# Kernel tuning notes

Measured on AMD Instinct MI355X. Metric: run time of the kernel, lower is better.

The kernel has to match this reference:

```python
import jax, jax.numpy as jnp
import numpy as np

NUM_HEADS = 16

def setup_inputs() -> dict:
    key = jax.random.key(0)
    ks = jax.random.split(key, 5)
    B, S, H = 16, 1025, 1024
    std = 0.02
    return {
        "hidden_states": jax.random.normal(ks[0], (B, S, H), jnp.float32),
        "w_qkv": jax.random.normal(ks[1], (3 * H, H), jnp.float32) * std,
        "b_qkv": jax.random.normal(ks[2], (3 * H,), jnp.float32) * std,
        "w_dense": jax.random.normal(ks[3], (H, H), jnp.float32) * std,
        "b_dense": jax.random.normal(ks[4], (H,), jnp.float32) * std,
    }

def reference(hidden_states, w_qkv, b_qkv, w_dense, b_dense):
    B, S, H = hidden_states.shape
    nh = NUM_HEADS
    hd = H // nh
    scale = hd ** -0.5
    # fused QKV projection: [B,S,3H]
    mixed = jnp.einsum('bsh,oh->bso', hidden_states, w_qkv) + b_qkv
    # reshape per torch: (B,S,nh,3,hd) -> permute(3,0,2,1,4)
    mixed = mixed.reshape(B, S, nh, 3, hd).transpose(3, 0, 2, 1, 4)
    q, k, v = mixed[0], mixed[1], mixed[2]          # each [B,nh,S,hd]
    scores = jnp.einsum('bhqd,bhkd->bhqk', q, k) * scale
    probs = jax.nn.softmax(scores, axis=-1)          # [B,nh,S,S]
    ctx = jnp.einsum('bhqk,bhkd->bhqd', probs, v)    # [B,nh,S,hd]
    ctx = ctx.transpose(0, 2, 1, 3).reshape(B, S, H)
    out = jnp.einsum('bsh,oh->bso', ctx, w_dense) + b_dense
    return out
```

## Files before the change

kernel.cpp:

```cpp
#include <hip/hip_runtime.h>
#include <math.h>

typedef float f32x4 __attribute__((ext_vector_type(4)));
typedef __bf16 bf16x8 __attribute__((ext_vector_type(8)));
typedef unsigned int u32;
typedef u32 u32x4 __attribute__((ext_vector_type(4)));

#define AS1 __attribute__((address_space(1)))
#define AS3 __attribute__((address_space(3)))

static __device__ __forceinline__ void gload16(const void* g, void* l) {
    __builtin_amdgcn_global_load_lds((const AS1 u32*)g, (AS3 u32*)l, 16, 0, 0);
}
static __device__ __forceinline__ f32x4 mfma16(bf16x8 a, bf16x8 b, f32x4 c) {
    return __builtin_amdgcn_mfma_f32_16x16x32_bf16(a, b, c, 0, 0, 0);
}
static __device__ __forceinline__ float exp2fast(float x) {
    return __builtin_amdgcn_exp2f(x);
}

__global__ __launch_bounds__(256)
void convert_kernel(const float* __restrict__ in, __bf16* __restrict__ out)
{
    const size_t i = ((size_t)blockIdx.x * 256 + threadIdx.x) * 8;
    f32x4 a = *(const f32x4*)(in + i);
    f32x4 b = *(const f32x4*)(in + i + 4);
    bf16x8 o;
    #pragma unroll
    for (int j = 0; j < 4; ++j) { o[j] = (__bf16)a[j]; o[j + 4] = (__bf16)b[j]; }
    *(bf16x8*)(out + i) = o;
}

template<int MODE>
__global__ __launch_bounds__(256)
void gemm_kernel(const __bf16* __restrict__ A, const __bf16* __restrict__ Bw,
                 const float* __restrict__ bias,
                 __bf16* __restrict__ q_out, __bf16* __restrict__ k_out,
                 __bf16* __restrict__ v_out, float* __restrict__ f_out)
{
    constexpr int M = 16400;
    constexpr int K = 1024;

    __shared__ __align__(16) __bf16 As[128 * 64];
    __shared__ __align__(16) __bf16 Bs[128 * 64];

    const int tid  = threadIdx.x;
    const int lane = tid & 63;
    const int wv   = tid >> 6;
    const int wr   = wv >> 1, wc = wv & 1;
    const int fr   = lane & 15, fq = lane >> 4;
    const int m0   = blockIdx.y * 128;
    const int n0   = blockIdx.x * 128;

    const __bf16* aptr[4];
    const __bf16* bptr[4];
    int loff[4];
    #pragma unroll
    for (int qd = 0; qd < 4; ++qd) {
        const int s  = qd * 256 + tid;
        const int r  = s >> 3;
        const int c  = (s & 7) ^ (r & 7);
        loff[qd] = s * 8;
        int ar = m0 + r; if (ar > M - 1) ar = M - 1;
        aptr[qd] = A  + (size_t)ar * K + c * 8;
        bptr[qd] = Bw + (size_t)(n0 + r) * K + c * 8;
    }

    f32x4 acc[4][4];
    #pragma unroll
    for (int i = 0; i < 4; ++i)
        #pragma unroll
        for (int j = 0; j < 4; ++j)
            acc[i][j] = f32x4{0.f, 0.f, 0.f, 0.f};

    for (int kt = 0; kt < K / 64; ++kt) {
        const int kof = kt * 64;
        #pragma unroll
        for (int qd = 0; qd < 4; ++qd) {
            gload16(aptr[qd] + kof, &As[loff[qd]]);
            gload16(bptr[qd] + kof, &Bs[loff[qd]]);
        }
        __syncthreads();

        #pragma unroll
        for (int ks = 0; ks < 2; ++ks) {
            bf16x8 a[4], b[4];
            #pragma unroll
            for (int i = 0; i < 4; ++i) {
                const int ra = wr * 64 + i * 16 + fr;
                const int rb = wc * 64 + i * 16 + fr;
                const int cg = ((ks * 4 + fq) ^ (fr & 7)) * 8;
                a[i] = *(const bf16x8*)&As[ra * 64 + cg];
                b[i] = *(const bf16x8*)&Bs[rb * 64 + cg];
            }
            #pragma unroll
            for (int i = 0; i < 4; ++i)
                #pragma unroll
                for (int j = 0; j < 4; ++j)
                    acc[i][j] = mfma16(a[i], b[j], acc[i][j]);
        }
        __syncthreads();
    }

    #pragma unroll
    for (int ni = 0; ni < 4; ++ni) {
        const int col = n0 + wc * 64 + ni * 16 + fr;
        const float bv = bias[col];
        if constexpr (MODE == 0) {
            const int head = col / 192;
            const int t    = (col >> 6) % 3;
            const int d    = col & 63;
            __bf16* dst = (t == 0) ? q_out : (t == 1 ? k_out : v_out);
            const float scale = (t == 0) ? 0.18033688011112042f : 1.0f;
            #pragma unroll
            for (int mi = 0; mi < 4; ++mi) {
                #pragma unroll
                for (int j = 0; j < 4; ++j) {
                    const int m = m0 + wr * 64 + mi * 16 + fq * 4 + j;
                    if (m < M) {
                        const int bb = m / 1025;
                        const int ss = m - bb * 1025;
                        dst[(((size_t)(bb * 16 + head)) * 1025 + ss) * 64 + d] =
                            (__bf16)((acc[mi][ni][j] + bv) * scale);
                    }
                }
            }
        } else {
            #pragma unroll
            for (int mi = 0; mi < 4; ++mi) {
                #pragma unroll
                for (int j = 0; j < 4; ++j) {
                    const int m = m0 + wr * 64 + mi * 16 + fq * 4 + j;
                    if (m < M) f_out[(size_t)m * 1024 + col] = acc[mi][ni][j] + bv;
                }
            }
        }
    }
}

__global__ __launch_bounds__(256)
void transpose_v(const __bf16* __restrict__ vb, __bf16* __restrict__ vt)
{
    constexpr int S = 1025, S2 = 1088;
    const int bh = blockIdx.y;
    const int s0 = blockIdx.x * 64;
    const int sr = threadIdx.x >> 2, sq = threadIdx.x & 3;
    int srow = s0 + sr; if (srow > S - 1) srow = S - 1;
    const __bf16* src = vb + ((size_t)bh * S + srow) * 64 + sq * 16;
    bf16x8 v0 = *(const bf16x8*)src;
    bf16x8 v1 = *(const bf16x8*)(src + 8);
    __bf16* dst = vt + (size_t)bh * 64 * S2 + s0 + sr;
    #pragma unroll
    for (int i = 0; i < 8; ++i) {
        dst[(size_t)(sq * 16 + i) * S2]     = v0[i];
        dst[(size_t)(sq * 16 + 8 + i) * S2] = v1[i];
    }
}

__global__ __launch_bounds__(256)
void attn_kernel(const __bf16* __restrict__ qb, const __bf16* __restrict__ kb,
                 const __bf16* __restrict__ vtb, __bf16* __restrict__ ctxb)
{
    constexpr int S = 1025, S2 = 1088;
    const int tid  = threadIdx.x;
    const int lane = tid & 63;
    const int w    = tid >> 6;
    const int fr   = lane & 15, fq = lane >> 4;
    const int bh   = blockIdx.y;
    const int q0   = blockIdx.x * 64;
    const int bb   = bh >> 4, hh = bh & 15;

    const __bf16* qp = qb  + (size_t)bh * S * 64;
    const __bf16* kp = kb  + (size_t)bh * S * 64;
    const __bf16* vp = vtb + (size_t)bh * 64 * S2;

    __shared__ __align__(16) __bf16 Ks[64 * 64];
    __shared__ __align__(16) __bf16 Vs[64 * 64];
    __shared__ u32 Ps[4][16 * 33];

    const int s0i = tid, s1i = tid + 256;
    const int r0 = s0i >> 3, g0 = (s0i & 7) ^ (r0 & 7);
    const int r1 = s1i >> 3, g1 = (s1i & 7) ^ (r1 & 7);
    const __bf16* vsrc0 = vp + (size_t)r0 * S2 + g0 * 8;
    const __bf16* vsrc1 = vp + (size_t)r1 * S2 + g1 * 8;

    int qrow = q0 + w * 16 + fr; if (qrow > S - 1) qrow = S - 1;
    const bf16x8 qa0 = *(const bf16x8*)(qp + (size_t)qrow * 64 + fq * 8);
    const bf16x8 qa1 = *(const bf16x8*)(qp + (size_t)qrow * 64 + 32 + fq * 8);

    f32x4 ctx[4];
    #pragma unroll
    for (int di = 0; di < 4; ++di) ctx[di] = f32x4{0.f, 0.f, 0.f, 0.f};
    float mrow = -1e30f;
    float lrow = 0.f;

    u32* psrow_w = &Ps[w][fr * 33];

    for (int kt = 0; kt < 17; ++kt) {
        const int kv0 = kt * 64;
        {
            int kr0 = kv0 + r0; if (kr0 > S - 1) kr0 = S - 1;
            int kr1 = kv0 + r1; if (kr1 > S - 1) kr1 = S - 1;
            gload16(kp + (size_t)kr0 * 64 + g0 * 8, &Ks[s0i * 8]);
            gload16(kp + (size_t)kr1 * 64 + g1 * 8, &Ks[s1i * 8]);
            gload16(vsrc0 + kv0, &Vs[s0i * 8]);
            gload16(vsrc1 + kv0, &Vs[s1i * 8]);
        }
        __syncthreads();

        f32x4 sc[4];
        #pragma unroll
        for (int ni = 0; ni < 4; ++ni) {
            const int row = ni * 16 + fr;
            bf16x8 kf0 = *(const bf16x8*)&Ks[row * 64 + ((fq    ) ^ (row & 7)) * 8];
            bf16x8 kf1 = *(const bf16x8*)&Ks[row * 64 + ((fq + 4) ^ (row & 7)) * 8];
            f32x4 z = f32x4{0.f, 0.f, 0.f, 0.f};
            z = mfma16(kf0, qa0, z);
            sc[ni] = mfma16(kf1, qa1, z);
        }
        if (kv0 + 64 > S) {
            #pragma unroll
            for (int ni = 0; ni < 4; ++ni)
                #pragma unroll
                for (int j = 0; j < 4; ++j)
                    if (kv0 + ni * 16 + fq * 4 + j >= S) sc[ni][j] = -1e30f;
        }

        float mt = sc[0][0];
        #pragma unroll
        for (int ni = 0; ni < 4; ++ni)
            #pragma unroll
            for (int j = 0; j < 4; ++j) mt = fmaxf(mt, sc[ni][j]);
        mt = fmaxf(mt, __shfl_xor(mt, 16, 64));
        mt = fmaxf(mt, __shfl_xor(mt, 32, 64));

        if (__any(mt > mrow + 8.0f)) {
            const float mnew = fmaxf(mrow, mt);
            const float alpha = exp2fast(mrow - mnew);
            mrow = mnew;
            lrow *= alpha;
            float a[4];
            #pragma unroll
            for (int j = 0; j < 4; ++j) a[j] = __shfl(alpha, fq * 4 + j, 64);
            #pragma unroll
            for (int di = 0; di < 4; ++di) {
                ctx[di][0] *= a[0]; ctx[di][1] *= a[1];
                ctx[di][2] *= a[2]; ctx[di][3] *= a[3];
            }
        }

        float p[4][4];
        float s = 0.f;
        #pragma unroll
        for (int ni = 0; ni < 4; ++ni)
            #pragma unroll
            for (int j = 0; j < 4; ++j) {
                p[ni][j] = exp2fast(sc[ni][j] - mrow);
                s += p[ni][j];
            }
        s += __shfl_xor(s, 16, 64);
        s += __shfl_xor(s, 32, 64);
        lrow += s;

        #pragma unroll
        for (int ni = 0; ni < 4; ++ni) {
            #pragma unroll
            for (int h = 0; h < 2; ++h) {
                unsigned short lo = __builtin_bit_cast(unsigned short, (__bf16)p[ni][2 * h]);
                unsigned short hi = __builtin_bit_cast(unsigned short, (__bf16)p[ni][2 * h + 1]);
                psrow_w[fq * 8 + ni * 2 + h] = (u32)lo | ((u32)hi << 16);
            }
        }
        u32x4 pav[2];
        #pragma unroll
        for (int ks = 0; ks < 2; ++ks)
            #pragma unroll
            for (int t = 0; t < 4; ++t) {
                const int slot = (2 * (fq & 1) + (t >> 1)) * 8
                               + (2 * ks + (fq >> 1)) * 2 + (t & 1);
                pav[ks][t] = psrow_w[slot];
            }

        #pragma unroll
        for (int ks = 0; ks < 2; ++ks) {
            const bf16x8 pa = __builtin_bit_cast(bf16x8, pav[ks]);
            #pragma unroll
            for (int di = 0; di < 4; ++di) {
                const int row = di * 16 + fr;
                bf16x8 vf = *(const bf16x8*)&Vs[row * 64 + ((ks * 4 + fq) ^ (row & 7)) * 8];
                ctx[di] = mfma16(pa, vf, ctx[di]);
            }
        }
        __syncthreads();
    }

    float linv[4];
    #pragma unroll
    for (int j = 0; j < 4; ++j) linv[j] = 1.0f / __shfl(lrow, fq * 4 + j, 64);
    #pragma unroll
    for (int di = 0; di < 4; ++di) {
        #pragma unroll
        for (int j = 0; j < 4; ++j) {
            const int qg = q0 + w * 16 + fq * 4 + j;
            if (qg < S) {
                ctxb[((size_t)bb * 1025 + qg) * 1024 + hh * 64 + di * 16 + fr] =
                    (__bf16)(ctx[di][j] * linv[j]);
            }
        }
    }
}

extern "C" void kernel_launch(void* const* d_in, const int* in_sizes, int n_in,
                              void* d_out, int out_size, void* d_ws, size_t ws_size,
                              hipStream_t stream)
{
    const float* hs      = (const float*)d_in[0];
    const float* w_qkv   = (const float*)d_in[1];
    const float* b_qkv   = (const float*)d_in[2];
    const float* w_dense = (const float*)d_in[3];
    const float* b_dense = (const float*)d_in[4];

    const size_t nHS = (size_t)16 * 1025 * 1024;
    const size_t nWQ = (size_t)3072 * 1024;
    const size_t nWD = (size_t)1024 * 1024;

    __bf16* hsb     = (__bf16*)d_ws;
    __bf16* wqkvb   = hsb + nHS;
    __bf16* wdenseb = wqkvb + nWQ;
    __bf16* qb      = wdenseb + nWD;
    __bf16* kb      = qb + nHS;
    __bf16* vb      = kb + nHS;
    __bf16* ctxb    = vb + nHS;
    __bf16* vtb     = ctxb + nHS;

    dim3 blk(256);
    convert_kernel<<<dim3((unsigned)(nHS / 2048)), blk, 0, stream>>>(hs, hsb);
    convert_kernel<<<dim3((unsigned)(nWQ / 2048)), blk, 0, stream>>>(w_qkv, wqkvb);
    convert_kernel<<<dim3((unsigned)(nWD / 2048)), blk, 0, stream>>>(w_dense, wdenseb);

    gemm_kernel<0><<<dim3(24, 129), blk, 0, stream>>>(
        hsb, wqkvb, b_qkv, qb, kb, vb, nullptr);

    transpose_v<<<dim3(17, 256), blk, 0, stream>>>(vb, vtb);

    attn_kernel<<<dim3(17, 256), blk, 0, stream>>>(qb, kb, vtb, ctxb);

    gemm_kernel<1><<<dim3(8, 129), blk, 0, stream>>>(
        ctxb, wdenseb, b_dense, nullptr, nullptr, nullptr, (float*)d_out);
}
```

Baseline: 454.0 us.

## Rewrite GEMM as 256x256 double-buffered 8-wave pipeline with XCD-aware block remap

```diff
diff --git a/kernel.cpp b/kernel.cpp
--- a/kernel.cpp
+++ b/kernel.cpp
@@ -32,7 +32,7 @@
 }
 
 template<int MODE>
-__global__ __launch_bounds__(256)
+__global__ __launch_bounds__(512, 2)
 void gemm_kernel(const __bf16* __restrict__ A, const __bf16* __restrict__ Bw,
                  const float* __restrict__ bias,
                  __bf16* __restrict__ q_out, __bf16* __restrict__ k_out,
@@ -40,67 +40,171 @@
 {
     constexpr int M = 16400;
     constexpr int K = 1024;
-
-    __shared__ __align__(16) __bf16 As[128 * 64];
-    __shared__ __align__(16) __bf16 Bs[128 * 64];
+    constexpr int NKT = 16;
+    constexpr int GX = (MODE == 0) ? 12 : 4;
+    constexpr int NWG = GX * 65;
+
+    __shared__ __align__(16) __bf16 ldsA[2][256 * 64];
+    __shared__ __align__(16) __bf16 ldsB[2][256 * 64];
 
     const int tid  = threadIdx.x;
     const int lane = tid & 63;
     const int wv   = tid >> 6;
-    const int wr   = wv >> 1, wc = wv & 1;
+    const int wr   = wv >> 2;
+    const int wc   = wv & 3;
     const int fr   = lane & 15, fq = lane >> 4;
-    const int m0   = blockIdx.y * 128;
-    const int n0   = blockIdx.x * 128;
-
-    const __bf16* aptr[4];
-    const __bf16* bptr[4];
-    int loff[4];
-    #pragma unroll
-    for (int qd = 0; qd < 4; ++qd) {
-        const int s  = qd * 256 + tid;
-        const int r  = s >> 3;
-        const int c  = (s & 7) ^ (r & 7);
-        loff[qd] = s * 8;
-        int ar = m0 + r; if (ar > M - 1) ar = M - 1;
-        aptr[qd] = A  + (size_t)ar * K + c * 8;
-        bptr[qd] = Bw + (size_t)(n0 + r) * K + c * 8;
-    }
-
-    f32x4 acc[4][4];
-    #pragma unroll
-    for (int i = 0; i < 4; ++i)
+
+    int flat = blockIdx.x;
+    {
+        constexpr int Q = NWG / 8, R = NWG % 8;
+        const int x = flat % 8, j = flat / 8;
+        flat = (x < R ? x * (Q + 1) : R * (Q + 1) + (x - R) * Q) + j;
+    }
+    const int bx = flat / 65, by = flat % 65;
+    const int m0 = by * 256, n0 = bx * 256;
+
+    const __bf16* aSrc[2][2]; int aDst[2][2];
+    #pragma unroll
+    for (int h = 0; h < 2; ++h)
+        #pragma unroll
+        for (int l = 0; l < 2; ++l) {
+            const int s   = l * 1024 + h * 512 + tid;
+            const int row = s >> 3, g = s & 7;
+            const int c   = g ^ (row & 7);
+            int m = m0 + row; if (m > M - 1) m = M - 1;
+            aSrc[h][l] = A + (size_t)m * K + c * 8;
+            aDst[h][l] = s * 8;
+        }
+    const __bf16* bSrc[2][2]; int bDst[2][2];
+    #pragma unroll
+    for (int n = 0; n < 2; ++n)
+        #pragma unroll
+        for (int l = 0; l < 2; ++l) {
+            const int q   = l * 2 + (tid >> 8);
+            const int p   = tid & 255;
+            const int row = q * 64 + n * 32 + (p >> 3);
+            const int g   = p & 7;
+            const int c   = g ^ (row & 7);
+            bSrc[n][l] = Bw + (size_t)(n0 + row) * K + c * 8;
+            bDst[n][l] = (row * 8 + g) * 8;
+        }
+
+#define STAGE_A(h, nb, ko) { \
+    gload16(aSrc[h][0] + (ko), &ldsA[nb][aDst[h][0]]); \
+    gload16(aSrc[h][1] + (ko), &ldsA[nb][aDst[h][1]]); }
+#define STAGE_B(n, nb, ko) { \
+    gload16(bSrc[n][0] + (ko), &ldsB[nb][bDst[n][0]]); \
+    gload16(bSrc[n][1] + (ko), &ldsB[nb][bDst[n][1]]); }
+
+    f32x4 acc[8][4];
+    #pragma unroll
+    for (int i = 0; i < 8; ++i)
         #pragma unroll
         for (int j = 0; j < 4; ++j)
             acc[i][j] = f32x4{0.f, 0.f, 0.f, 0.f};
 
-    for (int kt = 0; kt < K / 64; ++kt) {
-        const int kof = kt * 64;
-        #pragma unroll
-        for (int qd = 0; qd < 4; ++qd) {
-            gload16(aptr[qd] + kof, &As[loff[qd]]);
-            gload16(bptr[qd] + kof, &Bs[loff[qd]]);
-        }
-        __syncthreads();
-
-        #pragma unroll
-        for (int ks = 0; ks < 2; ++ks) {
-            bf16x8 a[4], b[4];
-            #pragma unroll
-            for (int i = 0; i < 4; ++i) {
-                const int ra = wr * 64 + i * 16 + fr;
-                const int rb = wc * 64 + i * 16 + fr;
-                const int cg = ((ks * 4 + fq) ^ (fr & 7)) * 8;
-                a[i] = *(const bf16x8*)&As[ra * 64 + cg];
-                b[i] = *(const bf16x8*)&Bs[rb * 64 + cg];
-            }
+    const int slot0 = ((0 + fq) ^ (fr & 7)) * 8;
+    const int slot1 = ((4 + fq) ^ (fr & 7)) * 8;
+    const int arow  = wr * 128 + fr;
+    const int brow  = wc * 64 + fr;
+
+    STAGE_A(0, 0, 0); STAGE_B(0, 0, 0); STAGE_B(1, 0, 0); STAGE_A(1, 0, 0);
+
+    for (int kt = 0; kt < NKT; ++kt) {
+        const int cur = kt & 1, nxt = cur ^ 1;
+        const int ko  = ((kt + 1 < NKT) ? kt + 1 : NKT - 1) * 64;
+        bf16x8 a[4][2], b[2][2];
+
+        STAGE_A(0, nxt, ko);
+        asm volatile("s_waitcnt vmcnt(6)" ::: "memory");
+        __builtin_amdgcn_s_barrier();
+        #pragma unroll
+        for (int i = 0; i < 4; ++i) {
+            a[i][0] = *(const bf16x8*)&ldsA[cur][(arow + i * 16) * 64 + slot0];
+            a[i][1] = *(const bf16x8*)&ldsA[cur][(arow + i * 16) * 64 + slot1];
+        }
+        #pragma unroll
+        for (int j = 0; j < 2; ++j) {
+            b[j][0] = *(const bf16x8*)&ldsB[cur][(brow + j * 16) * 64 + slot0];
+            b[j][1] = *(const bf16x8*)&ldsB[cur][(brow + j * 16) * 64 + slot1];
+        }
+        asm volatile("s_waitcnt lgkmcnt(0)" ::: "memory");
+        __builtin_amdgcn_sched_barrier(0);
+        __builtin_amdgcn_s_setprio(1);
+        #pragma unroll
+        for (int ks = 0; ks < 2; ++ks)
             #pragma unroll
             for (int i = 0; i < 4; ++i)
                 #pragma unroll
-                for (int j = 0; j < 4; ++j)
-                    acc[i][j] = mfma16(a[i], b[j], acc[i][j]);
-        }
-        __syncthreads();
-    }
+                for (int j = 0; j < 2; ++j)
+                    acc[i][j] = mfma16(a[i][ks], b[j][ks], acc[i][j]);
+        __builtin_amdgcn_s_setprio(0);
+
+        STAGE_B(0, nxt, ko);
+        asm volatile("s_waitcnt vmcnt(6)" ::: "memory");
+        __builtin_amdgcn_s_barrier();
+        #pragma unroll
+        for (int j = 0; j < 2; ++j) {
+            b[j][0] = *(const bf16x8*)&ldsB[cur][(brow + 32 + j * 16) * 64 + slot0];
+            b[j][1] = *(const bf16x8*)&ldsB[cur][(brow + 32 + j * 16) * 64 + slot1];
+        }
+        asm volatile("s_waitcnt lgkmcnt(0)" ::: "memory");
+        __builtin_amdgcn_sched_barrier(0);
+        __builtin_amdgcn_s_setprio(1);
+        #pragma unroll
+        for (int ks = 0; ks < 2; ++ks)
+            #pragma unroll
+            for (int i = 0; i < 4; ++i)
+                #pragma unroll
+                for (int j = 0; j < 2; ++j)
+                    acc[i][2 + j] = mfma16(a[i][ks], b[j][ks], acc[i][2 + j]);
+        __builtin_amdgcn_s_setprio(0);
+
+        STAGE_B(1, nxt, ko);
+        asm volatile("s_waitcnt vmcnt(6)" ::: "memory");
+        __builtin_amdgcn_s_barrier();
+        #pragma unroll
+        for (int i = 0; i < 4; ++i) {
+            a[i][0] = *(const bf16x8*)&ldsA[cur][(arow + 64 + i * 16) * 64 + slot0];
+            a[i][1] = *(const bf16x8*)&ldsA[cur][(arow + 64 + i * 16) * 64 + slot1];
+        }
+        #pragma unroll
+        for (int j = 0; j < 2; ++j) {
+            b[j][0] = *(const bf16x8*)&ldsB[cur][(brow + j * 16) * 64 + slot0];
+            b[j][1] = *(const bf16x8*)&ldsB[cur][(brow + j * 16) * 64 + slot1];
+        }
+        asm volatile("s_waitcnt lgkmcnt(0)" ::: "memory");
+        __builtin_amdgcn_sched_barrier(0);
+        __builtin_amdgcn_s_setprio(1);
+        #pragma unroll
+        for (int ks = 0; ks < 2; ++ks)
+            #pragma unroll
+            for (int i = 0; i < 4; ++i)
+                #pragma unroll
+                for (int j = 0; j < 2; ++j)
+                    acc[4 + i][j] = mfma16(a[i][ks], b[j][ks], acc[4 + i][j]);
+        __builtin_amdgcn_s_setprio(0);
+
+        STAGE_A(1, nxt, ko);
+        #pragma unroll
+        for (int j = 0; j < 2; ++j) {
+            b[j][0] = *(const bf16x8*)&ldsB[cur][(brow + 32 + j * 16) * 64 + slot0];
+            b[j][1] = *(const bf16x8*)&ldsB[cur][(brow + 32 + j * 16) * 64 + slot1];
+        }
+        asm volatile("s_waitcnt lgkmcnt(0)" ::: "memory");
+        __builtin_amdgcn_sched_barrier(0);
+        __builtin_amdgcn_s_setprio(1);
+        #pragma unroll
+        for (int ks = 0; ks < 2; ++ks)
+            #pragma unroll
+            for (int i = 0; i < 4; ++i)
+                #pragma unroll
+                for (int j = 0; j < 2; ++j)
+                    acc[4 + i][2 + j] = mfma16(a[i][ks], b[j][ks], acc[4 + i][2 + j]);
+        __builtin_amdgcn_s_setprio(0);
+        __builtin_amdgcn_s_barrier();
+    }
+    asm volatile("s_waitcnt vmcnt(0)" ::: "memory");
 
     #pragma unroll
     for (int ni = 0; ni < 4; ++ni) {
@@ -113,10 +217,10 @@
             __bf16* dst = (t == 0) ? q_out : (t == 1 ? k_out : v_out);
             const float scale = (t == 0) ? 0.18033688011112042f : 1.0f;
             #pragma unroll
-            for (int mi = 0; mi < 4; ++mi) {
+            for (int mi = 0; mi < 8; ++mi) {
                 #pragma unroll
                 for (int j = 0; j < 4; ++j) {
-                    const int m = m0 + wr * 64 + mi * 16 + fq * 4 + j;
+                    const int m = m0 + wr * 128 + mi * 16 + fq * 4 + j;
                     if (m < M) {
                         const int bb = m / 1025;
                         const int ss = m - bb * 1025;
@@ -127,15 +231,17 @@
             }
         } else {
             #pragma unroll
-            for (int mi = 0; mi < 4; ++mi) {
+            for (int mi = 0; mi < 8; ++mi) {
                 #pragma unroll
                 for (int j = 0; j < 4; ++j) {
-                    const int m = m0 + wr * 64 + mi * 16 + fq * 4 + j;
+                    const int m = m0 + wr * 128 + mi * 16 + fq * 4 + j;
                     if (m < M) f_out[(size_t)m * 1024 + col] = acc[mi][ni][j] + bv;
                 }
             }
         }
     }
+#undef STAGE_A
+#undef STAGE_B
 }
 
 __global__ __launch_bounds__(256)
@@ -338,13 +444,13 @@
     convert_kernel<<<dim3((unsigned)(nWQ / 2048)), blk, 0, stream>>>(w_qkv, wqkvb);
     convert_kernel<<<dim3((unsigned)(nWD / 2048)), blk, 0, stream>>>(w_dense, wdenseb);
 
-    gemm_kernel<0><<<dim3(24, 129), blk, 0, stream>>>(
+    gemm_kernel<0><<<dim3(12 * 65), dim3(512), 0, stream>>>(
         hsb, wqkvb, b_qkv, qb, kb, vb, nullptr);
 
     transpose_v<<<dim3(17, 256), blk, 0, stream>>>(vb, vtb);
 
     attn_kernel<<<dim3(17, 256), blk, 0, stream>>>(qb, kb, vtb, ctxb);
 
-    gemm_kernel<1><<<dim3(8, 129), blk, 0, stream>>>(
+    gemm_kernel<1><<<dim3(4 * 65), dim3(512), 0, stream>>>(
         ctxb, wdenseb, b_dense, nullptr, nullptr, nullptr, (float*)d_out);
 }
```

Measured after the change: 489.0 us. 1.08x slower.
